# Kernel tuning notes

Measured on AMD Instinct MI355X. Metric: run time of the kernel, lower is better.

## Reference

```python
import jax, jax.numpy as jnp
import numpy as np

B = 65536
STATE_DIM = 96
ACTION_DIM = 32
IN_FEATURES = STATE_DIM + ACTION_DIM  # 128
HIDDEN = 256
NUM_HEADS = 200
OUT_FEATURES = 1


def setup_inputs() -> dict:
    key = jax.random.key(0)
    ks = jax.random.split(key, 9)
    state = jax.random.normal(ks[0], (B, STATE_DIM), dtype=jnp.float32)
    action = jax.random.normal(ks[1], (B, ACTION_DIM), dtype=jnp.float32)
    alphas = jax.random.uniform(ks[2], (NUM_HEADS,), dtype=jnp.float32)
    W1 = jax.random.normal(ks[3], (HIDDEN, IN_FEATURES), dtype=jnp.float32) * 0.05
    b1 = jax.random.normal(ks[4], (HIDDEN,), dtype=jnp.float32) * 0.05
    W2 = jax.random.normal(ks[5], (HIDDEN, HIDDEN), dtype=jnp.float32) * 0.05
    b2 = jax.random.normal(ks[6], (HIDDEN,), dtype=jnp.float32) * 0.05
    # stacked head params: heads[h] is Linear(256 -> out_features)
    Wh = jax.random.normal(ks[7], (NUM_HEADS, OUT_FEATURES, HIDDEN), dtype=jnp.float32) * 0.05
    bh = jax.random.normal(ks[8], (NUM_HEADS, OUT_FEATURES), dtype=jnp.float32) * 0.05
    return {"state": state, "action": action, "alphas": alphas,
            "W1": W1, "b1": b1, "W2": W2, "b2": b2, "Wh": Wh, "bh": bh}


def reference(state, action, alphas, W1, b1, W2, b2, Wh, bh):
    x = jnp.concatenate([state, action], axis=1)          # [B, 128]
    x = jax.nn.relu(x @ W1.T + b1)                         # [B, 256]
    x = jax.nn.relu(x @ W2.T + b2)                         # [B, 256]
    # sum_h alpha_h * (x @ Wh[h].T + bh[h])  ==  x @ (sum_h alpha_h Wh[h]).T + sum_h alpha_h bh[h]
    Wc = jnp.einsum('h,hod->od', alphas, Wh)               # [out, 256]
    bc = jnp.einsum('h,ho->o', alphas, bh)                 # [out]
    return x @ Wc.T + bc                                   # [B, out]
```

## Files before the change

kernel.cpp:

```cpp
#include <hip/hip_runtime.h>
#include <hip/hip_bf16.h>


#define B_TOTAL 65536
#define SDIM 96
#define ADIM 32
#define IN_F 128
#define HID 256
#define NHEADS 200
#define BM 64
#define NTILES 4
#define XS_PITCH 132
#define H1_PITCH 260

typedef __bf16 bf16;
typedef __attribute__((ext_vector_type(4))) __bf16 bf16x4;
typedef __attribute__((ext_vector_type(8))) __bf16 bf16x8;
typedef __attribute__((ext_vector_type(4))) float f32x4;

__global__ void prep_kernel(const float* __restrict__ W1, const float* __restrict__ W2,
                            const float* __restrict__ alphas, const float* __restrict__ Wh,
                            const float* __restrict__ bh,
                            bf16* __restrict__ W1bf, bf16* __restrict__ W2bf,
                            float* __restrict__ Wc) {
    int tid = blockIdx.x * blockDim.x + threadIdx.x;
    if (tid < IN_F * HID) W1bf[tid] = (bf16)W1[tid];
    if (tid < HID * HID)  W2bf[tid] = (bf16)W2[tid];
    if (tid < HID) {
        float acc = 0.f;
        #pragma unroll 8
        for (int h = 0; h < NHEADS; ++h) acc += alphas[h] * Wh[h * HID + tid];
        Wc[tid] = acc;
    }
    if (tid == HID) {
        float acc = 0.f;
        for (int h = 0; h < NHEADS; ++h) acc += alphas[h] * bh[h];
        Wc[HID] = acc;
    }
}

__global__ __launch_bounds__(512, 2) void critic_kernel(
        const float* __restrict__ state, const float* __restrict__ action,
        const float* __restrict__ b1, const float* __restrict__ b2,
        const bf16* __restrict__ W1bf, const bf16* __restrict__ W2bf,
        const float* __restrict__ Wc, float* __restrict__ out) {

    __shared__ bf16 xs[BM * XS_PITCH];
    __shared__ bf16 h1s[BM * H1_PITCH];
    __shared__ float sPart[8][BM];

    const int tid  = threadIdx.x;
    const int wave = tid >> 6;
    const int lane = tid & 63;
    const int q    = lane >> 4;
    const int ln   = lane & 15;
    const int colw = wave * 32;
    const int brow0 = blockIdx.x * (BM * NTILES);

    bf16x8 w1f[4][2];
    #pragma unroll
    for (int ks = 0; ks < 4; ++ks)
        #pragma unroll
        for (int nt = 0; nt < 2; ++nt)
            w1f[ks][nt] = *(const bf16x8*)&W1bf[(size_t)(colw + nt * 16 + ln) * IN_F + ks * 32 + q * 8];

    bf16x8 w2f[8][2];
    #pragma unroll
    for (int ks = 0; ks < 8; ++ks)
        #pragma unroll
        for (int nt = 0; nt < 2; ++nt)
            w2f[ks][nt] = *(const bf16x8*)&W2bf[(size_t)(colw + nt * 16 + ln) * HID + ks * 32 + q * 8];

    f32x4 b1v[2], b2v[2], wcv[2];
    #pragma unroll
    for (int nt = 0; nt < 2; ++nt) {
        const int n4 = colw + nt * 16 + q * 4;
        b1v[nt] = *(const f32x4*)&b1[n4];
        b2v[nt] = *(const f32x4*)&b2[n4];
        wcv[nt] = *(const f32x4*)&Wc[n4];
    }
    const float bc = Wc[HID];

    float4 px[2][2];
    #pragma unroll
    for (int i = 0; i < 2; ++i) {
        const int c  = tid + i * 512;
        const int r  = c >> 4;
        const int c8 = c & 15;
        const float* src = (c8 < 12) ? (state  + (size_t)(brow0 + r) * SDIM + c8 * 8)
                                     : (action + (size_t)(brow0 + r) * ADIM + (c8 - 12) * 8);
        px[i][0] = ((const float4*)src)[0];
        px[i][1] = ((const float4*)src)[1];
    }

    for (int t = 0; t < NTILES; ++t) {
        const int row0 = brow0 + t * BM;

        #pragma unroll
        for (int i = 0; i < 2; ++i) {
            const int c  = tid + i * 512;
            const int r  = c >> 4;
            const int c8 = c & 15;
            bf16x8 v = (bf16x8){(bf16)px[i][0].x, (bf16)px[i][0].y, (bf16)px[i][0].z, (bf16)px[i][0].w,
                                (bf16)px[i][1].x, (bf16)px[i][1].y, (bf16)px[i][1].z, (bf16)px[i][1].w};
            *(bf16x8*)&xs[r * XS_PITCH + c8 * 8] = v;
        }
        __syncthreads();

        if (t + 1 < NTILES) {
            const int nrow0 = row0 + BM;
            #pragma unroll
            for (int i = 0; i < 2; ++i) {
                const int c  = tid + i * 512;
                const int r  = c >> 4;
                const int c8 = c & 15;
                const float* src = (c8 < 12) ? (state  + (size_t)(nrow0 + r) * SDIM + c8 * 8)
                                             : (action + (size_t)(nrow0 + r) * ADIM + (c8 - 12) * 8);
                px[i][0] = ((const float4*)src)[0];
                px[i][1] = ((const float4*)src)[1];
            }
        }

        f32x4 acc[4][2];
        #pragma unroll
        for (int mt = 0; mt < 4; ++mt)
            #pragma unroll
            for (int nt = 0; nt < 2; ++nt)
                acc[mt][nt] = (f32x4){0.f, 0.f, 0.f, 0.f};

        #pragma unroll
        for (int ks = 0; ks < 4; ++ks) {
            const int k0 = ks * 32 + q * 8;
            bf16x8 bfr[4];
            #pragma unroll
            for (int mt = 0; mt < 4; ++mt)
                bfr[mt] = *(const bf16x8*)&xs[(mt * 16 + ln) * XS_PITCH + k0];
            #pragma unroll
            for (int mt = 0; mt < 4; ++mt)
                #pragma unroll
                for (int nt = 0; nt < 2; ++nt)
                    acc[mt][nt] = __builtin_amdgcn_mfma_f32_16x16x32_bf16(w1f[ks][nt], bfr[mt], acc[mt][nt], 0, 0, 0);
        }

        #pragma unroll
        for (int nt = 0; nt < 2; ++nt) {
            #pragma unroll
            for (int mt = 0; mt < 4; ++mt) {
                bf16x4 v4;
                #pragma unroll
                for (int r = 0; r < 4; ++r) {
                    float v = acc[mt][nt][r] + b1v[nt][r];
                    v = v > 0.f ? v : 0.f;
                    v4[r] = (bf16)v;
                }
                *(bf16x4*)&h1s[(mt * 16 + ln) * H1_PITCH + colw + nt * 16 + q * 4] = v4;
            }
        }
        __syncthreads();

        #pragma unroll
        for (int mt = 0; mt < 4; ++mt)
            #pragma unroll
            for (int nt = 0; nt < 2; ++nt)
                acc[mt][nt] = (f32x4){0.f, 0.f, 0.f, 0.f};

        #pragma unroll
        for (int ks = 0; ks < 8; ++ks) {
            const int k0 = ks * 32 + q * 8;
            bf16x8 bfr[4];
            #pragma unroll
            for (int mt = 0; mt < 4; ++mt)
                bfr[mt] = *(const bf16x8*)&h1s[(mt * 16 + ln) * H1_PITCH + k0];
            #pragma unroll
            for (int mt = 0; mt < 4; ++mt)
                #pragma unroll
                for (int nt = 0; nt < 2; ++nt)
                    acc[mt][nt] = __builtin_amdgcn_mfma_f32_16x16x32_bf16(w2f[ks][nt], bfr[mt], acc[mt][nt], 0, 0, 0);
        }

        float partial[4];
        #pragma unroll
        for (int mt = 0; mt < 4; ++mt) {
            float p = 0.f;
            #pragma unroll
            for (int nt = 0; nt < 2; ++nt)
                #pragma unroll
                for (int r = 0; r < 4; ++r) {
                    float v = acc[mt][nt][r] + b2v[nt][r];
                    v = v > 0.f ? v : 0.f;
                    p += v * wcv[nt][r];
                }
            partial[mt] = p;
        }
        #pragma unroll
        for (int mt = 0; mt < 4; ++mt) {
            partial[mt] += __shfl_xor(partial[mt], 16, 64);
            partial[mt] += __shfl_xor(partial[mt], 32, 64);
        }
        if (q == 0) {
            #pragma unroll
            for (int mt = 0; mt < 4; ++mt)
                sPart[wave][mt * 16 + ln] = partial[mt];
        }
        __syncthreads();

        if (tid < BM) {
            float v = bc;
            #pragma unroll
            for (int w = 0; w < 8; ++w) v += sPart[w][tid];
            out[row0 + tid] = v;
        }
    }
}

extern "C" void kernel_launch(void* const* d_in, const int* in_sizes, int n_in,
                              void* d_out, int out_size, void* d_ws, size_t ws_size,
                              hipStream_t stream) {
    const float* state  = (const float*)d_in[0];
    const float* action = (const float*)d_in[1];
    const float* alphas = (const float*)d_in[2];
    const float* W1     = (const float*)d_in[3];
    const float* b1     = (const float*)d_in[4];
    const float* W2     = (const float*)d_in[5];
    const float* b2     = (const float*)d_in[6];
    const float* Wh     = (const float*)d_in[7];
    const float* bh     = (const float*)d_in[8];
    float* out = (float*)d_out;

    bf16*  W1bf = (bf16*)d_ws;
    bf16*  W2bf = (bf16*)((char*)d_ws + 65536);
    float* Wc   = (float*)((char*)d_ws + 65536 + 131072);

    prep_kernel<<<256, 256, 0, stream>>>(W1, W2, alphas, Wh, bh, W1bf, W2bf, Wc);
    critic_kernel<<<B_TOTAL / (BM * NTILES), 512, 0, stream>>>(state, action, b1, b2, W1bf, W2bf, Wc, out);
}
```

Baseline: 111.1 us.

## Software-pipeline layer1 and layer2 across tiles with double-buffered LDS

Restructures the per-tile loop into a skewed pipeline: in each iteration, layer 1 of tile t and layer 2 of tile t-1 run together, and the output reduction of tile t-2 is written. The x, h1 and partial-sum LDS buffers are double-buffered, which cuts the barrier count per tile from three to one. The aim is to overlap MFMA work from both layers and remove synchronisation stalls. In exchange LDS use roughly doubles (~100KB via dynamic shared memory), which may limit residency to one block per CU, and register pressure grows.

```diff
diff --git a/kernel.cpp b/kernel.cpp
--- a/kernel.cpp
+++ b/kernel.cpp
@@ -12,6 +12,9 @@
 #define NTILES 4
 #define XS_PITCH 132
 #define H1_PITCH 260
+#define XS_ELEMS (BM * XS_PITCH)
+#define H1_ELEMS (BM * H1_PITCH)
+#define SMEM_BYTES (2 * XS_ELEMS * 2 + 2 * H1_ELEMS * 2 + 2 * 8 * BM * 4)
 
 typedef __bf16 bf16;
 typedef __attribute__((ext_vector_type(4))) __bf16 bf16x4;
@@ -45,9 +48,10 @@
         const bf16* __restrict__ W1bf, const bf16* __restrict__ W2bf,
         const float* __restrict__ Wc, float* __restrict__ out) {
 
-    __shared__ bf16 xs[BM * XS_PITCH];
-    __shared__ bf16 h1s[BM * H1_PITCH];
-    __shared__ float sPart[8][BM];
+    extern __shared__ char smem[];
+    bf16*  xs    = (bf16*)smem;
+    bf16*  h1s   = (bf16*)(smem + 2 * XS_ELEMS * 2);
+    float* sPart = (float*)(smem + 2 * XS_ELEMS * 2 + 2 * H1_ELEMS * 2);
 
     const int tid  = threadIdx.x;
     const int wave = tid >> 6;
@@ -82,134 +86,164 @@
     const float bc = Wc[HID];
 
     float4 px[2][2];
-    #pragma unroll
-    for (int i = 0; i < 2; ++i) {
-        const int c  = tid + i * 512;
-        const int r  = c >> 4;
-        const int c8 = c & 15;
-        const float* src = (c8 < 12) ? (state  + (size_t)(brow0 + r) * SDIM + c8 * 8)
-                                     : (action + (size_t)(brow0 + r) * ADIM + (c8 - 12) * 8);
-        px[i][0] = ((const float4*)src)[0];
-        px[i][1] = ((const float4*)src)[1];
-    }
-
-    for (int t = 0; t < NTILES; ++t) {
-        const int row0 = brow0 + t * BM;
-
+    const int c0r  = tid >> 4;
+    const int c0c8 = tid & 15;
+    const int c1r  = (tid + 512) >> 4;
+    const int c1c8 = (tid + 512) & 15;
+
+    {
+        const float* s0 = (c0c8 < 12) ? (state  + (size_t)(brow0 + c0r) * SDIM + c0c8 * 8)
+                                      : (action + (size_t)(brow0 + c0r) * ADIM + (c0c8 - 12) * 8);
+        const float* s1 = (c1c8 < 12) ? (state  + (size_t)(brow0 + c1r) * SDIM + c1c8 * 8)
+                                      : (action + (size_t)(brow0 + c1r) * ADIM + (c1c8 - 12) * 8);
+        px[0][0] = ((const float4*)s0)[0]; px[0][1] = ((const float4*)s0)[1];
+        px[1][0] = ((const float4*)s1)[0]; px[1][1] = ((const float4*)s1)[1];
+        bf16x8 v0 = (bf16x8){(bf16)px[0][0].x, (bf16)px[0][0].y, (bf16)px[0][0].z, (bf16)px[0][0].w,
+                             (bf16)px[0][1].x, (bf16)px[0][1].y, (bf16)px[0][1].z, (bf16)px[0][1].w};
+        bf16x8 v1 = (bf16x8){(bf16)px[1][0].x, (bf16)px[1][0].y, (bf16)px[1][0].z, (bf16)px[1][0].w,
+                             (bf16)px[1][1].x, (bf16)px[1][1].y, (bf16)px[1][1].z, (bf16)px[1][1].w};
+        *(bf16x8*)&xs[c0r * XS_PITCH + c0c8 * 8] = v0;
+        *(bf16x8*)&xs[c1r * XS_PITCH + c1c8 * 8] = v1;
+        const int n0 = brow0 + BM;
+        const float* t0 = (c0c8 < 12) ? (state  + (size_t)(n0 + c0r) * SDIM + c0c8 * 8)
+                                      : (action + (size_t)(n0 + c0r) * ADIM + (c0c8 - 12) * 8);
+        const float* t1 = (c1c8 < 12) ? (state  + (size_t)(n0 + c1r) * SDIM + c1c8 * 8)
+                                      : (action + (size_t)(n0 + c1r) * ADIM + (c1c8 - 12) * 8);
+        px[0][0] = ((const float4*)t0)[0]; px[0][1] = ((const float4*)t0)[1];
+        px[1][0] = ((const float4*)t1)[0]; px[1][1] = ((const float4*)t1)[1];
+    }
+    __syncthreads();
+
+    #pragma unroll
+    for (int t = 0; t <= NTILES; ++t) {
+        if (t < NTILES) {
+            const bf16* xsb = xs  + (t & 1) * XS_ELEMS;
+            bf16*       h1b = h1s + (t & 1) * H1_ELEMS;
+
+            f32x4 acc1[4][2];
+            #pragma unroll
+            for (int mt = 0; mt < 4; ++mt)
+                #pragma unroll
+                for (int nt = 0; nt < 2; ++nt)
+                    acc1[mt][nt] = (f32x4){0.f, 0.f, 0.f, 0.f};
+
+            #pragma unroll
+            for (int ks = 0; ks < 4; ++ks) {
+                const int k0 = ks * 32 + q * 8;
+                bf16x8 bfr[4];
+                #pragma unroll
+                for (int mt = 0; mt < 4; ++mt)
+                    bfr[mt] = *(const bf16x8*)&xsb[(mt * 16 + ln) * XS_PITCH + k0];
+                #pragma unroll
+                for (int mt = 0; mt < 4; ++mt)
+                    #pragma unroll
+                    for (int nt = 0; nt < 2; ++nt)
+                        acc1[mt][nt] = __builtin_amdgcn_mfma_f32_16x16x32_bf16(w1f[ks][nt], bfr[mt], acc1[mt][nt], 0, 0, 0);
+            }
+            #pragma unroll
+            for (int nt = 0; nt < 2; ++nt)
+                #pragma unroll
+                for (int mt = 0; mt < 4; ++mt) {
+                    bf16x4 v4;
+                    #pragma unroll
+                    for (int r = 0; r < 4; ++r) {
+                        float v = acc1[mt][nt][r] + b1v[nt][r];
+                        v = v > 0.f ? v : 0.f;
+                        v4[r] = (bf16)v;
+                    }
+                    *(bf16x4*)&h1b[(mt * 16 + ln) * H1_PITCH + colw + nt * 16 + q * 4] = v4;
+                }
+
+            if (t + 1 < NTILES) {
+                bf16* xsn = xs + ((t + 1) & 1) * XS_ELEMS;
+                bf16x8 v0 = (bf16x8){(bf16)px[0][0].x, (bf16)px[0][0].y, (bf16)px[0][0].z, (bf16)px[0][0].w,
+                                     (bf16)px[0][1].x, (bf16)px[0][1].y, (bf16)px[0][1].z, (bf16)px[0][1].w};
+                bf16x8 v1 = (bf16x8){(bf16)px[1][0].x, (bf16)px[1][0].y, (bf16)px[1][0].z, (bf16)px[1][0].w,
+                                     (bf16)px[1][1].x, (bf16)px[1][1].y, (bf16)px[1][1].z, (bf16)px[1][1].w};
+                *(bf16x8*)&xsn[c0r * XS_PITCH + c0c8 * 8] = v0;
+                *(bf16x8*)&xsn[c1r * XS_PITCH + c1c8 * 8] = v1;
+            }
+            if (t + 2 < NTILES) {
+                const int n0 = brow0 + (t + 2) * BM;
+                const float* t0 = (c0c8 < 12) ? (state  + (size_t)(n0 + c0r) * SDIM + c0c8 * 8)
+                                              : (action + (size_t)(n0 + c0r) * ADIM + (c0c8 - 12) * 8);
+                const float* t1 = (c1c8 < 12) ? (state  + (size_t)(n0 + c1r) * SDIM + c1c8 * 8)
+                                              : (action + (size_t)(n0 + c1r) * ADIM + (c1c8 - 12) * 8);
+                px[0][0] = ((const float4*)t0)[0]; px[0][1] = ((const float4*)t0)[1];
+                px[1][0] = ((const float4*)t1)[0]; px[1][1] = ((const float4*)t1)[1];
+            }
+        }
+
+        if (t >= 1) {
+            const bf16* h1b = h1s + ((t - 1) & 1) * H1_ELEMS;
+
+            f32x4 acc2[4][2];
+            #pragma unroll
+            for (int mt = 0; mt < 4; ++mt)
+                #pragma unroll
+                for (int nt = 0; nt < 2; ++nt)
+                    acc2[mt][nt] = (f32x4){0.f, 0.f, 0.f, 0.f};
+
+            #pragma unroll
+            for (int ks = 0; ks < 8; ++ks) {
+                const int k0 = ks * 32 + q * 8;
+                bf16x8 bfr[4];
+                #pragma unroll
+                for (int mt = 0; mt < 4; ++mt)
+                    bfr[mt] = *(const bf16x8*)&h1b[(mt * 16 + ln) * H1_PITCH + k0];
+                #pragma unroll
+                for (int mt = 0; mt < 4; ++mt)
+                    #pragma unroll
+                    for (int nt = 0; nt < 2; ++nt)
+                        acc2[mt][nt] = __builtin_amdgcn_mfma_f32_16x16x32_bf16(w2f[ks][nt], bfr[mt], acc2[mt][nt], 0, 0, 0);
+            }
+
+            float partial[4];
+            #pragma unroll
+            for (int mt = 0; mt < 4; ++mt) {
+                float p = 0.f;
+                #pragma unroll
+                for (int nt = 0; nt < 2; ++nt)
+                    #pragma unroll
+                    for (int r = 0; r < 4; ++r) {
+                        float v = acc2[mt][nt][r] + b2v[nt][r];
+                        v = v > 0.f ? v : 0.f;
+                        p += v * wcv[nt][r];
+                    }
+                partial[mt] = p;
+            }
+            #pragma unroll
+            for (int mt = 0; mt < 4; ++mt) {
+                partial[mt] += __shfl_xor(partial[mt], 16, 64);
+                partial[mt] += __shfl_xor(partial[mt], 32, 64);
+            }
+            if (q == 0) {
+                float* sp = sPart + ((t - 1) & 1) * (8 * BM) + wave * BM;
+                #pragma unroll
+                for (int mt = 0; mt < 4; ++mt)
+                    sp[mt * 16 + ln] = partial[mt];
+            }
+        }
+
+        if (t >= 2) {
+            if (tid < BM) {
+                const float* sp = sPart + ((t - 2) & 1) * (8 * BM);
+                float v = bc;
+                #pragma unroll
+                for (int w = 0; w < 8; ++w) v += sp[w * BM + tid];
+                out[brow0 + (t - 2) * BM + tid] = v;
+            }
+        }
+
+        __syncthreads();
+    }
+
+    if (tid < BM) {
+        const float* sp = sPart + ((NTILES - 1) & 1) * (8 * BM);
+        float v = bc;
         #pragma unroll
-        for (int i = 0; i < 2; ++i) {
-            const int c  = tid + i * 512;
-            const int r  = c >> 4;
-            const int c8 = c & 15;
-            bf16x8 v = (bf16x8){(bf16)px[i][0].x, (bf16)px[i][0].y, (bf16)px[i][0].z, (bf16)px[i][0].w,
-                                (bf16)px[i][1].x, (bf16)px[i][1].y, (bf16)px[i][1].z, (bf16)px[i][1].w};
-            *(bf16x8*)&xs[r * XS_PITCH + c8 * 8] = v;
-        }
-        __syncthreads();
-
-        if (t + 1 < NTILES) {
-            const int nrow0 = row0 + BM;
-            #pragma unroll
-            for (int i = 0; i < 2; ++i) {
-                const int c  = tid + i * 512;
-                const int r  = c >> 4;
-                const int c8 = c & 15;
-                const float* src = (c8 < 12) ? (state  + (size_t)(nrow0 + r) * SDIM + c8 * 8)
-                                             : (action + (size_t)(nrow0 + r) * ADIM + (c8 - 12) * 8);
-                px[i][0] = ((const float4*)src)[0];
-                px[i][1] = ((const float4*)src)[1];
-            }
-        }
-
-        f32x4 acc[4][2];
-        #pragma unroll
-        for (int mt = 0; mt < 4; ++mt)
-            #pragma unroll
-            for (int nt = 0; nt < 2; ++nt)
-                acc[mt][nt] = (f32x4){0.f, 0.f, 0.f, 0.f};
-
-        #pragma unroll
-        for (int ks = 0; ks < 4; ++ks) {
-            const int k0 = ks * 32 + q * 8;
-            bf16x8 bfr[4];
-            #pragma unroll
-            for (int mt = 0; mt < 4; ++mt)
-                bfr[mt] = *(const bf16x8*)&xs[(mt * 16 + ln) * XS_PITCH + k0];
-            #pragma unroll
-            for (int mt = 0; mt < 4; ++mt)
-                #pragma unroll
-                for (int nt = 0; nt < 2; ++nt)
-                    acc[mt][nt] = __builtin_amdgcn_mfma_f32_16x16x32_bf16(w1f[ks][nt], bfr[mt], acc[mt][nt], 0, 0, 0);
-        }
-
-        #pragma unroll
-        for (int nt = 0; nt < 2; ++nt) {
-            #pragma unroll
-            for (int mt = 0; mt < 4; ++mt) {
-                bf16x4 v4;
-                #pragma unroll
-                for (int r = 0; r < 4; ++r) {
-                    float v = acc[mt][nt][r] + b1v[nt][r];
-                    v = v > 0.f ? v : 0.f;
-                    v4[r] = (bf16)v;
-                }
-                *(bf16x4*)&h1s[(mt * 16 + ln) * H1_PITCH + colw + nt * 16 + q * 4] = v4;
-            }
-        }
-        __syncthreads();
-
-        #pragma unroll
-        for (int mt = 0; mt < 4; ++mt)
-            #pragma unroll
-            for (int nt = 0; nt < 2; ++nt)
-                acc[mt][nt] = (f32x4){0.f, 0.f, 0.f, 0.f};
-
-        #pragma unroll
-        for (int ks = 0; ks < 8; ++ks) {
-            const int k0 = ks * 32 + q * 8;
-            bf16x8 bfr[4];
-            #pragma unroll
-            for (int mt = 0; mt < 4; ++mt)
-                bfr[mt] = *(const bf16x8*)&h1s[(mt * 16 + ln) * H1_PITCH + k0];
-            #pragma unroll
-            for (int mt = 0; mt < 4; ++mt)
-                #pragma unroll
-                for (int nt = 0; nt < 2; ++nt)
-                    acc[mt][nt] = __builtin_amdgcn_mfma_f32_16x16x32_bf16(w2f[ks][nt], bfr[mt], acc[mt][nt], 0, 0, 0);
-        }
-
-        float partial[4];
-        #pragma unroll
-        for (int mt = 0; mt < 4; ++mt) {
-            float p = 0.f;
-            #pragma unroll
-            for (int nt = 0; nt < 2; ++nt)
-                #pragma unroll
-                for (int r = 0; r < 4; ++r) {
-                    float v = acc[mt][nt][r] + b2v[nt][r];
-                    v = v > 0.f ? v : 0.f;
-                    p += v * wcv[nt][r];
-                }
-            partial[mt] = p;
-        }
-        #pragma unroll
-        for (int mt = 0; mt < 4; ++mt) {
-            partial[mt] += __shfl_xor(partial[mt], 16, 64);
-            partial[mt] += __shfl_xor(partial[mt], 32, 64);
-        }
-        if (q == 0) {
-            #pragma unroll
-            for (int mt = 0; mt < 4; ++mt)
-                sPart[wave][mt * 16 + ln] = partial[mt];
-        }
-        __syncthreads();
-
-        if (tid < BM) {
-            float v = bc;
-            #pragma unroll
-            for (int w = 0; w < 8; ++w) v += sPart[w][tid];
-            out[row0 + tid] = v;
-        }
+        for (int w = 0; w < 8; ++w) v += sp[w * BM + tid];
+        out[brow0 + (NTILES - 1) * BM + tid] = v;
     }
 }
 
@@ -231,6 +265,12 @@
     bf16*  W2bf = (bf16*)((char*)d_ws + 65536);
     float* Wc   = (float*)((char*)d_ws + 65536 + 131072);
 
+    static bool attr_done = false;
+    (void)hipFuncSetAttribute((const void*)critic_kernel,
+                              hipFuncAttributeMaxDynamicSharedMemorySize,
+                              SMEM_BYTES);
+
     prep_kernel<<<256, 256, 0, stream>>>(W1, W2, alphas, Wh, bh, W1bf, W2bf, Wc);
-    critic_kernel<<<B_TOTAL / (BM * NTILES), 512, 0, stream>>>(state, action, b1, b2, W1bf, W2bf, Wc, out);
+    critic_kernel<<<B_TOTAL / (BM * NTILES), 512, SMEM_BYTES, stream>>>(
+        state, action, b1, b2, W1bf, W2bf, Wc, out);
 }
```

After: 145.5 us. 30.9% more time.

## Restructure tile pipeline with double-buffered partials and fewer tiles per block

Applied to the files above, without the earlier changes.

Halves the number of row tiles per block, doubling the grid. The loop is restructured so each iteration has two barriers instead of three. The next tile's input is loaded after the layer-1 barrier and written to shared memory during layer-2 epilogue. Partial sums are double-buffered, and the final reduction of the previous tile is deferred into the next iteration. The goal is to cut barrier count and improve occupancy, at the cost of loading weights into registers twice as often across blocks.

```diff
diff --git a/kernel.cpp b/kernel.cpp
--- a/kernel.cpp
+++ b/kernel.cpp
@@ -9,7 +9,7 @@
 #define HID 256
 #define NHEADS 200
 #define BM 64
-#define NTILES 4
+#define NTILES 2
 #define XS_PITCH 132
 #define H1_PITCH 260
 
@@ -47,7 +47,7 @@
 
     __shared__ bf16 xs[BM * XS_PITCH];
     __shared__ bf16 h1s[BM * H1_PITCH];
-    __shared__ float sPart[8][BM];
+    __shared__ float sPart[2][8][BM];
 
     const int tid  = threadIdx.x;
     const int wave = tid >> 6;
@@ -81,44 +81,34 @@
     }
     const float bc = Wc[HID];
 
-    float4 px[2][2];
-    #pragma unroll
-    for (int i = 0; i < 2; ++i) {
-        const int c  = tid + i * 512;
-        const int r  = c >> 4;
-        const int c8 = c & 15;
-        const float* src = (c8 < 12) ? (state  + (size_t)(brow0 + r) * SDIM + c8 * 8)
-                                     : (action + (size_t)(brow0 + r) * ADIM + (c8 - 12) * 8);
-        px[i][0] = ((const float4*)src)[0];
-        px[i][1] = ((const float4*)src)[1];
-    }
+    const int c0r  = tid >> 4;
+    const int c0c8 = tid & 15;
+    const int c1r  = (tid + 512) >> 4;
+    const int c1c8 = (tid + 512) & 15;
+
+    {
+        const float* s0 = (c0c8 < 12) ? (state  + (size_t)(brow0 + c0r) * SDIM + c0c8 * 8)
+                                      : (action + (size_t)(brow0 + c0r) * ADIM + (c0c8 - 12) * 8);
+        const float* s1 = (c1c8 < 12) ? (state  + (size_t)(brow0 + c1r) * SDIM + c1c8 * 8)
+                                      : (action + (size_t)(brow0 + c1r) * ADIM + (c1c8 - 12) * 8);
+        float4 a0 = ((const float4*)s0)[0], a1 = ((const float4*)s0)[1];
+        float4 b0 = ((const float4*)s1)[0], b1_ = ((const float4*)s1)[1];
+        *(bf16x8*)&xs[c0r * XS_PITCH + c0c8 * 8] =
+            (bf16x8){(bf16)a0.x, (bf16)a0.y, (bf16)a0.z, (bf16)a0.w,
+                     (bf16)a1.x, (bf16)a1.y, (bf16)a1.z, (bf16)a1.w};
+        *(bf16x8*)&xs[c1r * XS_PITCH + c1c8 * 8] =
+            (bf16x8){(bf16)b0.x, (bf16)b0.y, (bf16)b0.z, (bf16)b0.w,
+                     (bf16)b1_.x, (bf16)b1_.y, (bf16)b1_.z, (bf16)b1_.w};
+    }
+    __syncthreads();
 
     for (int t = 0; t < NTILES; ++t) {
-        const int row0 = brow0 + t * BM;
-
-        #pragma unroll
-        for (int i = 0; i < 2; ++i) {
-            const int c  = tid + i * 512;
-            const int r  = c >> 4;
-            const int c8 = c & 15;
-            bf16x8 v = (bf16x8){(bf16)px[i][0].x, (bf16)px[i][0].y, (bf16)px[i][0].z, (bf16)px[i][0].w,
-                                (bf16)px[i][1].x, (bf16)px[i][1].y, (bf16)px[i][1].z, (bf16)px[i][1].w};
-            *(bf16x8*)&xs[r * XS_PITCH + c8 * 8] = v;
-        }
-        __syncthreads();
-
-        if (t + 1 < NTILES) {
-            const int nrow0 = row0 + BM;
-            #pragma unroll
-            for (int i = 0; i < 2; ++i) {
-                const int c  = tid + i * 512;
-                const int r  = c >> 4;
-                const int c8 = c & 15;
-                const float* src = (c8 < 12) ? (state  + (size_t)(nrow0 + r) * SDIM + c8 * 8)
-                                             : (action + (size_t)(nrow0 + r) * ADIM + (c8 - 12) * 8);
-                px[i][0] = ((const float4*)src)[0];
-                px[i][1] = ((const float4*)src)[1];
-            }
+        if (t >= 1 && tid < BM) {
+            const float (*sp)[BM] = sPart[(t - 1) & 1];
+            float v = bc;
+            #pragma unroll
+            for (int w = 0; w < 8; ++w) v += sp[w][tid];
+            out[brow0 + (t - 1) * BM + tid] = v;
         }
 
         f32x4 acc[4][2];
@@ -141,9 +131,8 @@
                 for (int nt = 0; nt < 2; ++nt)
                     acc[mt][nt] = __builtin_amdgcn_mfma_f32_16x16x32_bf16(w1f[ks][nt], bfr[mt], acc[mt][nt], 0, 0, 0);
         }
-
-        #pragma unroll
-        for (int nt = 0; nt < 2; ++nt) {
+        #pragma unroll
+        for (int nt = 0; nt < 2; ++nt)
             #pragma unroll
             for (int mt = 0; mt < 4; ++mt) {
                 bf16x4 v4;
@@ -155,8 +144,19 @@
                 }
                 *(bf16x4*)&h1s[(mt * 16 + ln) * H1_PITCH + colw + nt * 16 + q * 4] = v4;
             }
-        }
         __syncthreads();
+
+        float4 pxa0, pxa1, pxb0, pxb1;
+        const bool have_next = (t + 1 < NTILES);
+        if (have_next) {
+            const int n0 = brow0 + (t + 1) * BM;
+            const float* s0 = (c0c8 < 12) ? (state  + (size_t)(n0 + c0r) * SDIM + c0c8 * 8)
+                                          : (action + (size_t)(n0 + c0r) * ADIM + (c0c8 - 12) * 8);
+            const float* s1 = (c1c8 < 12) ? (state  + (size_t)(n0 + c1r) * SDIM + c1c8 * 8)
+                                          : (action + (size_t)(n0 + c1r) * ADIM + (c1c8 - 12) * 8);
+            pxa0 = ((const float4*)s0)[0]; pxa1 = ((const float4*)s0)[1];
+            pxb0 = ((const float4*)s1)[0]; pxb1 = ((const float4*)s1)[1];
+        }
 
         #pragma unroll
         for (int mt = 0; mt < 4; ++mt)
@@ -200,16 +200,26 @@
         if (q == 0) {
             #pragma unroll
             for (int mt = 0; mt < 4; ++mt)
-                sPart[wave][mt * 16 + ln] = partial[mt];
+                sPart[t & 1][wave][mt * 16 + ln] = partial[mt];
+        }
+
+        if (have_next) {
+            *(bf16x8*)&xs[c0r * XS_PITCH + c0c8 * 8] =
+                (bf16x8){(bf16)pxa0.x, (bf16)pxa0.y, (bf16)pxa0.z, (bf16)pxa0.w,
+                         (bf16)pxa1.x, (bf16)pxa1.y, (bf16)pxa1.z, (bf16)pxa1.w};
+            *(bf16x8*)&xs[c1r * XS_PITCH + c1c8 * 8] =
+                (bf16x8){(bf16)pxb0.x, (bf16)pxb0.y, (bf16)pxb0.z, (bf16)pxb0.w,
+                         (bf16)pxb1.x, (bf16)pxb1.y, (bf16)pxb1.z, (bf16)pxb1.w};
         }
         __syncthreads();
-
-        if (tid < BM) {
-            float v = bc;
-            #pragma unroll
-            for (int w = 0; w < 8; ++w) v += sPart[w][tid];
-            out[row0 + tid] = v;
-        }
+    }
+
+    if (tid < BM) {
+        const float (*sp)[BM] = sPart[(NTILES - 1) & 1];
+        float v = bc;
+        #pragma unroll
+        for (int w = 0; w < 8; ++w) v += sp[w][tid];
+        out[brow0 + (NTILES - 1) * BM + tid] = v;
     }
 }
 
@@ -232,5 +242,6 @@
     float* Wc   = (float*)((char*)d_ws + 65536 + 131072);
 
     prep_kernel<<<256, 256, 0, stream>>>(W1, W2, alphas, Wh, bh, W1bf, W2bf, Wc);
-    critic_kernel<<<B_TOTAL / (BM * NTILES), 512, 0, stream>>>(state, action, b1, b2, W1bf, W2bf, Wc, out);
+    critic_kernel<<<B_TOTAL / (BM * NTILES), 512, 0, stream>>>(
+        state, action, b1, b2, W1bf, W2bf, Wc, out);
 }
```

After: 119.6 us. 1.08x slower.

## Fuse weight prep into critic kernel, removing separate prep launch

Applied to the files above, without the earlier changes.

Drops the prep kernel. Each block now converts W1/W2 from fp32 to bf16 in registers as it loads them, and computes the alpha-weighted head combination into shared memory. This removes one kernel launch and the workspace round trip. In exchange, every one of the 256 blocks redundantly reads the fp32 weights (twice the bytes) and all 200 heads of Wh, and asm pins are added to keep the packed weights in registers.

```diff
diff --git a/kernel.cpp b/kernel.cpp
--- a/kernel.cpp
+++ b/kernel.cpp
@@ -18,36 +18,34 @@
 typedef __attribute__((ext_vector_type(8))) __bf16 bf16x8;
 typedef __attribute__((ext_vector_type(4))) float f32x4;
 
-__global__ void prep_kernel(const float* __restrict__ W1, const float* __restrict__ W2,
-                            const float* __restrict__ alphas, const float* __restrict__ Wh,
-                            const float* __restrict__ bh,
-                            bf16* __restrict__ W1bf, bf16* __restrict__ W2bf,
-                            float* __restrict__ Wc) {
-    int tid = blockIdx.x * blockDim.x + threadIdx.x;
-    if (tid < IN_F * HID) W1bf[tid] = (bf16)W1[tid];
-    if (tid < HID * HID)  W2bf[tid] = (bf16)W2[tid];
-    if (tid < HID) {
-        float acc = 0.f;
-        #pragma unroll 8
-        for (int h = 0; h < NHEADS; ++h) acc += alphas[h] * Wh[h * HID + tid];
-        Wc[tid] = acc;
-    }
-    if (tid == HID) {
-        float acc = 0.f;
-        for (int h = 0; h < NHEADS; ++h) acc += alphas[h] * bh[h];
-        Wc[HID] = acc;
-    }
+static __device__ __forceinline__ float4 pack_bf16x8_as_f4(float4 a, float4 b) {
+    union { bf16x8 h; float4 f; } u;
+    u.h = (bf16x8){(bf16)a.x, (bf16)a.y, (bf16)a.z, (bf16)a.w,
+                   (bf16)b.x, (bf16)b.y, (bf16)b.z, (bf16)b.w};
+    return u.f;
+}
+static __device__ __forceinline__ bf16x8 as_bf16x8(float4 v) {
+    union { float4 f; bf16x8 h; } u;
+    u.f = v;
+    return u.h;
+}
+static __device__ __forceinline__ void pin_f4(float4& v) {
+    asm volatile("" : "+v"(v.x), "+v"(v.y), "+v"(v.z), "+v"(v.w));
 }
 
 __global__ __launch_bounds__(512, 2) void critic_kernel(
         const float* __restrict__ state, const float* __restrict__ action,
-        const float* __restrict__ b1, const float* __restrict__ b2,
-        const bf16* __restrict__ W1bf, const bf16* __restrict__ W2bf,
-        const float* __restrict__ Wc, float* __restrict__ out) {
-
-    __shared__ bf16 xs[BM * XS_PITCH];
-    __shared__ bf16 h1s[BM * H1_PITCH];
+        const float* __restrict__ alphas,
+        const float* __restrict__ W1, const float* __restrict__ b1,
+        const float* __restrict__ W2, const float* __restrict__ b2,
+        const float* __restrict__ Wh, const float* __restrict__ bh,
+        float* __restrict__ out) {
+
+    __shared__ bf16  xs[BM * XS_PITCH];
+    __shared__ bf16  h1s[BM * H1_PITCH];
     __shared__ float sPart[8][BM];
+    __shared__ float sWcP[2][HID];
+    __shared__ float sWc[HID + 1];
 
     const int tid  = threadIdx.x;
     const int wave = tid >> 6;
@@ -57,68 +55,104 @@
     const int colw = wave * 32;
     const int brow0 = blockIdx.x * (BM * NTILES);
 
-    bf16x8 w1f[4][2];
+    float4 w1s[4][2];
     #pragma unroll
     for (int ks = 0; ks < 4; ++ks)
         #pragma unroll
-        for (int nt = 0; nt < 2; ++nt)
-            w1f[ks][nt] = *(const bf16x8*)&W1bf[(size_t)(colw + nt * 16 + ln) * IN_F + ks * 32 + q * 8];
-
-    bf16x8 w2f[8][2];
+        for (int nt = 0; nt < 2; ++nt) {
+            const float* p = W1 + (size_t)(colw + nt * 16 + ln) * IN_F + ks * 32 + q * 8;
+            w1s[ks][nt] = pack_bf16x8_as_f4(((const float4*)p)[0], ((const float4*)p)[1]);
+        }
+
+    float4 w2s[8][2];
     #pragma unroll
     for (int ks = 0; ks < 8; ++ks)
         #pragma unroll
-        for (int nt = 0; nt < 2; ++nt)
-            w2f[ks][nt] = *(const bf16x8*)&W2bf[(size_t)(colw + nt * 16 + ln) * HID + ks * 32 + q * 8];
-
-    f32x4 b1v[2], b2v[2], wcv[2];
+        for (int nt = 0; nt < 2; ++nt) {
+            const float* p = W2 + (size_t)(colw + nt * 16 + ln) * HID + ks * 32 + q * 8;
+            w2s[ks][nt] = pack_bf16x8_as_f4(((const float4*)p)[0], ((const float4*)p)[1]);
+        }
+
+    #pragma unroll
+    for (int ks = 0; ks < 4; ++ks)
+        #pragma unroll
+        for (int nt = 0; nt < 2; ++nt)
+            pin_f4(w1s[ks][nt]);
+    #pragma unroll
+    for (int ks = 0; ks < 8; ++ks)
+        #pragma unroll
+        for (int nt = 0; nt < 2; ++nt)
+            pin_f4(w2s[ks][nt]);
+
+    f32x4 b1v[2], b2v[2];
     #pragma unroll
     for (int nt = 0; nt < 2; ++nt) {
         const int n4 = colw + nt * 16 + q * 4;
         b1v[nt] = *(const f32x4*)&b1[n4];
         b2v[nt] = *(const f32x4*)&b2[n4];
-        wcv[nt] = *(const f32x4*)&Wc[n4];
-    }
-    const float bc = Wc[HID];
+    }
+
+    {
+        const int c    = tid & 255;
+        const int half = tid >> 8;
+        float p = 0.f;
+        #pragma unroll 10
+        for (int i = 0; i < 100; ++i) {
+            const int h = half * 100 + i;
+            p += alphas[h] * Wh[(size_t)h * HID + c];
+        }
+        sWcP[half][c] = p;
+    }
+    if (tid < 64) {
+        float p = 0.f;
+        #pragma unroll
+        for (int i = 0; i < 4; ++i) {
+            const int h = tid + i * 64;
+            if (h < NHEADS) p += alphas[h] * bh[h];
+        }
+        #pragma unroll
+        for (int off = 1; off < 64; off <<= 1)
+            p += __shfl_xor(p, off, 64);
+        if (tid == 0) sWc[HID] = p;
+    }
+
+    const int c0r  = tid >> 4;
+    const int c0c8 = tid & 15;
+    const int c1r  = (tid + 512) >> 4;
+    const int c1c8 = (tid + 512) & 15;
 
     float4 px[2][2];
-    #pragma unroll
-    for (int i = 0; i < 2; ++i) {
-        const int c  = tid + i * 512;
-        const int r  = c >> 4;
-        const int c8 = c & 15;
-        const float* src = (c8 < 12) ? (state  + (size_t)(brow0 + r) * SDIM + c8 * 8)
-                                     : (action + (size_t)(brow0 + r) * ADIM + (c8 - 12) * 8);
-        px[i][0] = ((const float4*)src)[0];
-        px[i][1] = ((const float4*)src)[1];
+    {
+        const float* s0 = (c0c8 < 12) ? (state  + (size_t)(brow0 + c0r) * SDIM + c0c8 * 8)
+                                      : (action + (size_t)(brow0 + c0r) * ADIM + (c0c8 - 12) * 8);
+        const float* s1 = (c1c8 < 12) ? (state  + (size_t)(brow0 + c1r) * SDIM + c1c8 * 8)
+                                      : (action + (size_t)(brow0 + c1r) * ADIM + (c1c8 - 12) * 8);
+        px[0][0] = ((const float4*)s0)[0]; px[0][1] = ((const float4*)s0)[1];
+        px[1][0] = ((const float4*)s1)[0]; px[1][1] = ((const float4*)s1)[1];
     }
 
     for (int t = 0; t < NTILES; ++t) {
         const int row0 = brow0 + t * BM;
 
-        #pragma unroll
-        for (int i = 0; i < 2; ++i) {
-            const int c  = tid + i * 512;
-            const int r  = c >> 4;
-            const int c8 = c & 15;
-            bf16x8 v = (bf16x8){(bf16)px[i][0].x, (bf16)px[i][0].y, (bf16)px[i][0].z, (bf16)px[i][0].w,
-                                (bf16)px[i][1].x, (bf16)px[i][1].y, (bf16)px[i][1].z, (bf16)px[i][1].w};
-            *(bf16x8*)&xs[r * XS_PITCH + c8 * 8] = v;
-        }
+        *(bf16x8*)&xs[c0r * XS_PITCH + c0c8 * 8] =
+            (bf16x8){(bf16)px[0][0].x, (bf16)px[0][0].y, (bf16)px[0][0].z, (bf16)px[0][0].w,
+                     (bf16)px[0][1].x, (bf16)px[0][1].y, (bf16)px[0][1].z, (bf16)px[0][1].w};
+        *(bf16x8*)&xs[c1r * XS_PITCH + c1c8 * 8] =
+            (bf16x8){(bf16)px[1][0].x, (bf16)px[1][0].y, (bf16)px[1][0].z, (bf16)px[1][0].w,
+                     (bf16)px[1][1].x, (bf16)px[1][1].y, (bf16)px[1][1].z, (bf16)px[1][1].w};
         __syncthreads();
 
+        if (t == 0 && tid < HID)
+            sWc[tid] = sWcP[0][tid] + sWcP[1][tid];
+
         if (t + 1 < NTILES) {
-            const int nrow0 = row0 + BM;
-            #pragma unroll
-            for (int i = 0; i < 2; ++i) {
-                const int c  = tid + i * 512;
-                const int r  = c >> 4;
-                const int c8 = c & 15;
-                const float* src = (c8 < 12) ? (state  + (size_t)(nrow0 + r) * SDIM + c8 * 8)
-                                             : (action + (size_t)(nrow0 + r) * ADIM + (c8 - 12) * 8);
-                px[i][0] = ((const float4*)src)[0];
-                px[i][1] = ((const float4*)src)[1];
-            }
+            const int n0 = row0 + BM;
+            const float* s0 = (c0c8 < 12) ? (state  + (size_t)(n0 + c0r) * SDIM + c0c8 * 8)
+                                          : (action + (size_t)(n0 + c0r) * ADIM + (c0c8 - 12) * 8);
+            const float* s1 = (c1c8 < 12) ? (state  + (size_t)(n0 + c1r) * SDIM + c1c8 * 8)
+                                          : (action + (size_t)(n0 + c1r) * ADIM + (c1c8 - 12) * 8);
+            px[0][0] = ((const float4*)s0)[0]; px[0][1] = ((const float4*)s0)[1];
+            px[1][0] = ((const float4*)s1)[0]; px[1][1] = ((const float4*)s1)[1];
         }
 
         f32x4 acc[4][2];
@@ -139,11 +173,11 @@
             for (int mt = 0; mt < 4; ++mt)
                 #pragma unroll
                 for (int nt = 0; nt < 2; ++nt)
-                    acc[mt][nt] = __builtin_amdgcn_mfma_f32_16x16x32_bf16(w1f[ks][nt], bfr[mt], acc[mt][nt], 0, 0, 0);
-        }
-
-        #pragma unroll
-        for (int nt = 0; nt < 2; ++nt) {
+                    acc[mt][nt] = __builtin_amdgcn_mfma_f32_16x16x32_bf16(
+                        as_bf16x8(w1s[ks][nt]), bfr[mt], acc[mt][nt], 0, 0, 0);
+        }
+        #pragma unroll
+        for (int nt = 0; nt < 2; ++nt)
             #pragma unroll
             for (int mt = 0; mt < 4; ++mt) {
                 bf16x4 v4;
@@ -155,7 +189,6 @@
                 }
                 *(bf16x4*)&h1s[(mt * 16 + ln) * H1_PITCH + colw + nt * 16 + q * 4] = v4;
             }
-        }
         __syncthreads();
 
         #pragma unroll
@@ -175,8 +208,14 @@
             for (int mt = 0; mt < 4; ++mt)
                 #pragma unroll
                 for (int nt = 0; nt < 2; ++nt)
-                    acc[mt][nt] = __builtin_amdgcn_mfma_f32_16x16x32_bf16(w2f[ks][nt], bfr[mt], acc[mt][nt], 0, 0, 0);
-        }
+                    acc[mt][nt] = __builtin_amdgcn_mfma_f32_16x16x32_bf16(
+                        as_bf16x8(w2s[ks][nt]), bfr[mt], acc[mt][nt], 0, 0, 0);
+        }
+
+        f32x4 wcv[2];
+        #pragma unroll
+        for (int nt = 0; nt < 2; ++nt)
+            wcv[nt] = *(const f32x4*)&sWc[colw + nt * 16 + q * 4];
 
         float partial[4];
         #pragma unroll
@@ -205,7 +244,7 @@
         __syncthreads();
 
         if (tid < BM) {
-            float v = bc;
+            float v = sWc[HID];
             #pragma unroll
             for (int w = 0; w < 8; ++w) v += sPart[w][tid];
             out[row0 + tid] = v;
@@ -227,10 +266,6 @@
     const float* bh     = (const float*)d_in[8];
     float* out = (float*)d_out;
 
-    bf16*  W1bf = (bf16*)d_ws;
-    bf16*  W2bf = (bf16*)((char*)d_ws + 65536);
-    float* Wc   = (float*)((char*)d_ws + 65536 + 131072);
-
-    prep_kernel<<<256, 256, 0, stream>>>(W1, W2, alphas, Wh, bh, W1bf, W2bf, Wc);
-    critic_kernel<<<B_TOTAL / (BM * NTILES), 512, 0, stream>>>(state, action, b1, b2, W1bf, W2bf, Wc, out);
-}
+    critic_kernel<<<B_TOTAL / (BM * NTILES), 512, 0, stream>>>(
+        state, action, alphas, W1, b1, W2, b2, Wh, bh, out);
+}
```

New measurement: 112.5 us. No clear change (+1.2%).
